# Kernel optimization log

Measured on AMD Instinct MI355X. Metric: run time of the kernel, lower is better.

Reference implementation:

```python
import jax, jax.numpy as jnp
import numpy as np

EPS = 1e-7  # Keras K.epsilon()


def setup_inputs() -> dict:
    key = jax.random.key(0)
    k_x, k_w, k_b, k_u = jax.random.split(key, 4)
    B, T, D, A = 256, 512, 256, 50
    x = jax.random.normal(k_x, (B, T, D), dtype=jnp.float32)
    # Keras initializers.get('normal') -> stddev 0.05 RandomNormal
    W = jax.random.normal(k_w, (D, A), dtype=jnp.float32) * 0.05
    b = jax.random.normal(k_b, (A,), dtype=jnp.float32) * 0.05
    u = jax.random.normal(k_u, (A, 1), dtype=jnp.float32) * 0.05
    return {"x": x, "W": W, "b": b, "u": u}


def reference(x, W, b, u):
    # uit: [B, T, A]
    uit = jnp.tanh(jnp.einsum('btd,da->bta', x, W) + b)
    # ait: [B, T] raw scores -> exp-normalize (as in original, no max-subtract)
    ait = jnp.einsum('bta,a->bt', uit, u[:, 0])
    ait = jnp.exp(ait)
    ait = ait / (jnp.sum(ait, axis=1, keepdims=True) + EPS)
    # weighted pool over time: [B, D]
    return jnp.einsum('btd,bt->bd', x, ait)
```

## Files before the change

### kernel.cpp

```cpp
#include <hip/hip_runtime.h>
#include <math.h>

#define B_  256
#define T_  512
#define D_  256
#define A_  50
#define EPS 1e-7f

typedef short  short8  __attribute__((ext_vector_type(8)));
typedef float  floatx4 __attribute__((ext_vector_type(4)));

__device__ inline unsigned short f2bf(float f) {
    unsigned int u = __float_as_uint(f);
    u = (u + 0x7fffu + ((u >> 16) & 1u)) >> 16;
    return (unsigned short)u;
}

__global__ void prep_kernel(const float* __restrict__ W,
                            const float* __restrict__ bias,
                            const float* __restrict__ u,
                            unsigned short* __restrict__ Wf,
                            float* __restrict__ bu64)
{
    int idx = blockIdx.x * 256 + threadIdx.x;
    int j  = idx & 7;
    int l  = (idx >> 3) & 63;
    int ks = (idx >> 9) & 7;
    int nt = idx >> 12;
    int n  = nt * 16 + (l & 15);
    int k  = ks * 32 + (l >> 4) * 8 + j;
    float val = (n < A_) ? W[k * A_ + n] : 0.0f;
    Wf[idx] = f2bf(val);
    if (idx < 64) {
        bu64[idx]      = (idx < A_) ? bias[idx] : 0.0f;
        bu64[64 + idx] = (idx < A_) ? u[idx]    : 0.0f;
    }
}

__global__ __launch_bounds__(256)
void scores_kernel(const float* __restrict__ x,
                   const unsigned short* __restrict__ Wf,
                   const float* __restrict__ bu64,
                   float* __restrict__ s_out, float* __restrict__ partial)
{
    __shared__ float sred[64];

    const int tid  = threadIdx.x;
    const int w    = tid >> 6;
    const int l    = tid & 63;
    const int c    = l & 15;
    const int quad = l >> 4;
    const size_t rowbase = (size_t)blockIdx.x * 64 + w * 16;

    const float4* __restrict__ xrow = (const float4*)(x + (rowbase + c) * D_);
    const short8* __restrict__ wf8  = (const short8*)Wf;

    float bnc[4], unc[4];
    #pragma unroll
    for (int nt = 0; nt < 4; nt++) {
        bnc[nt] = bu64[nt * 16 + c];
        unc[nt] = bu64[64 + nt * 16 + c];
    }

    floatx4 acc[4];
    #pragma unroll
    for (int nt = 0; nt < 4; nt++) acc[nt] = (floatx4){0.f, 0.f, 0.f, 0.f};

    #pragma unroll
    for (int ks = 0; ks < 8; ks++) {
        const float4 a0 = xrow[ks * 8 + quad * 2];
        const float4 a1 = xrow[ks * 8 + quad * 2 + 1];
        short8 av;
        av[0] = (short)f2bf(a0.x); av[1] = (short)f2bf(a0.y);
        av[2] = (short)f2bf(a0.z); av[3] = (short)f2bf(a0.w);
        av[4] = (short)f2bf(a1.x); av[5] = (short)f2bf(a1.y);
        av[6] = (short)f2bf(a1.z); av[7] = (short)f2bf(a1.w);
        #pragma unroll
        for (int nt = 0; nt < 4; nt++) {
            const short8 bv = wf8[(nt * 8 + ks) * 64 + l];
            acc[nt] = __builtin_amdgcn_mfma_f32_16x16x32_bf16(av, bv, acc[nt], 0, 0, 0);
        }
    }

    float part[4];
    #pragma unroll
    for (int r = 0; r < 4; r++) {
        float v = 0.0f;
        #pragma unroll
        for (int nt = 0; nt < 4; nt++)
            v += tanhf(acc[nt][r] + bnc[nt]) * unc[nt];
        #pragma unroll
        for (int off = 1; off < 16; off <<= 1)
            v += __shfl_xor(v, off, 16);
        part[r] = v;
    }

    if (c == 0) {
        #pragma unroll
        for (int r = 0; r < 4; r++) {
            const float s = expf(part[r]);
            s_out[rowbase + quad * 4 + r] = s;
            sred[w * 16 + quad * 4 + r] = s;
        }
    }
    __syncthreads();
    if (tid == 0) {
        float s = 0.0f;
        #pragma unroll
        for (int i = 0; i < 64; i++) s += sred[i];
        partial[blockIdx.x] = s;
    }
}

__global__ __launch_bounds__(256)
void pool_kernel(const float* __restrict__ x, const float* __restrict__ s_in,
                 const float* __restrict__ partial, float* __restrict__ pp)
{
    __shared__ float s_lds[64];
    __shared__ float part[4 * 256];

    const int tid = threadIdx.x;
    const int bb  = blockIdx.x >> 3;
    const int q   = blockIdx.x & 7;

    float den = EPS;
    #pragma unroll
    for (int i = 0; i < 8; i++) den += partial[bb * 8 + i];
    const float inv = 1.0f / den;

    if (tid < 64)
        s_lds[tid] = s_in[(size_t)bb * T_ + q * 64 + tid] * inv;
    __syncthreads();

    const int w = tid >> 6;
    const int l = tid & 63;

    const float* __restrict__ xb = x + ((size_t)bb * T_ + q * 64) * D_;
    float4 acc = make_float4(0.f, 0.f, 0.f, 0.f);

    #pragma unroll
    for (int i = 0; i < 16; i++) {
        const int t = w * 16 + i;
        float4 xv = *(const float4*)(xb + (size_t)t * D_ + l * 4);
        float sv  = s_lds[t];
        acc.x += xv.x * sv;
        acc.y += xv.y * sv;
        acc.z += xv.z * sv;
        acc.w += xv.w * sv;
    }

    part[w * 256 + l * 4 + 0] = acc.x;
    part[w * 256 + l * 4 + 1] = acc.y;
    part[w * 256 + l * 4 + 2] = acc.z;
    part[w * 256 + l * 4 + 3] = acc.w;
    __syncthreads();

    pp[(size_t)blockIdx.x * 256 + tid] =
        part[tid] + part[256 + tid] + part[512 + tid] + part[768 + tid];
}

__global__ __launch_bounds__(256)
void combine_kernel(const float* __restrict__ pp, float* __restrict__ out)
{
    const size_t idx = (size_t)blockIdx.x * 256 + threadIdx.x;
    const size_t b   = idx >> 8;
    const size_t d   = idx & 255;
    float o = 0.0f;
    #pragma unroll
    for (int q = 0; q < 8; q++) o += pp[(b * 8 + q) * 256 + d];
    out[idx] = o;
}

extern "C" void kernel_launch(void* const* d_in, const int* in_sizes, int n_in,
                              void* d_out, int out_size, void* d_ws, size_t ws_size,
                              hipStream_t stream)
{
    const float* x = (const float*)d_in[0];
    const float* W = (const float*)d_in[1];
    const float* b = (const float*)d_in[2];
    const float* u = (const float*)d_in[3];

    float* scores  = (float*)d_ws;
    float* partial = scores + (size_t)B_ * T_;
    float* bu64    = partial + 2048;
    float* pp      = bu64 + 128;
    unsigned short* Wf = (unsigned short*)(pp + (size_t)B_ * 8 * 256);
    float* out     = (float*)d_out;

    prep_kernel   <<<64,   256, 0, stream>>>(W, b, u, Wf, bu64);
    scores_kernel <<<2048, 256, 0, stream>>>(x, Wf, bu64, scores, partial);
    pool_kernel   <<<2048, 256, 0, stream>>>(x, scores, partial, pp);
    combine_kernel<<<B_,   256, 0, stream>>>(pp, out);
}
```

Measured before the change: 224.4 us.

## Fuse scores, softmax normalization and pooling into one per-batch kernel

Replaces the scores, pool and combine kernels with a single 1024-thread block per batch row. The block computes the attention scores into LDS, reduces the denominator in-block, and pools x while the batch slice is likely still cache-resident. This removes the intermediate score and partial buffers and two launches. In exchange the grid shrinks to 256 blocks, which lowers parallelism, and it adds a serial LDS tree reduction.

```diff
diff --git a/kernel.cpp b/kernel.cpp
--- a/kernel.cpp
+++ b/kernel.cpp
@@ -6,6 +6,7 @@
 #define D_  256
 #define A_  50
 #define EPS 1e-7f
+#define NW  16
 
 typedef short  short8  __attribute__((ext_vector_type(8)));
 typedef float  floatx4 __attribute__((ext_vector_type(4)));
@@ -37,23 +38,24 @@
     }
 }
 
-__global__ __launch_bounds__(256)
-void scores_kernel(const float* __restrict__ x,
-                   const unsigned short* __restrict__ Wf,
-                   const float* __restrict__ bu64,
-                   float* __restrict__ s_out, float* __restrict__ partial)
+__global__ __launch_bounds__(1024)
+void fused_kernel(const float* __restrict__ x,
+                  const unsigned short* __restrict__ Wf,
+                  const float* __restrict__ bu64,
+                  float* __restrict__ out)
 {
-    __shared__ float sred[64];
+    __shared__ float s_lds[T_];
+    __shared__ float part[NW * 256];
 
     const int tid  = threadIdx.x;
     const int w    = tid >> 6;
     const int l    = tid & 63;
     const int c    = l & 15;
     const int quad = l >> 4;
-    const size_t rowbase = (size_t)blockIdx.x * 64 + w * 16;
+    const int bb   = blockIdx.x;
 
-    const float4* __restrict__ xrow = (const float4*)(x + (rowbase + c) * D_);
-    const short8* __restrict__ wf8  = (const short8*)Wf;
+    const float*  __restrict__ xb  = x + (size_t)bb * T_ * D_;
+    const short8* __restrict__ wf8 = (const short8*)Wf;
 
     float bnc[4], unc[4];
     #pragma unroll
@@ -62,113 +64,81 @@
         unc[nt] = bu64[64 + nt * 16 + c];
     }
 
-    floatx4 acc[4];
     #pragma unroll
-    for (int nt = 0; nt < 4; nt++) acc[nt] = (floatx4){0.f, 0.f, 0.f, 0.f};
+    for (int pass = 0; pass < 2; pass++) {
+        const int rowbase = pass * 256 + w * 16;
+        const float4* __restrict__ xrow =
+            (const float4*)(xb + (size_t)(rowbase + c) * D_);
 
-    #pragma unroll
-    for (int ks = 0; ks < 8; ks++) {
-        const float4 a0 = xrow[ks * 8 + quad * 2];
-        const float4 a1 = xrow[ks * 8 + quad * 2 + 1];
-        short8 av;
-        av[0] = (short)f2bf(a0.x); av[1] = (short)f2bf(a0.y);
-        av[2] = (short)f2bf(a0.z); av[3] = (short)f2bf(a0.w);
-        av[4] = (short)f2bf(a1.x); av[5] = (short)f2bf(a1.y);
-        av[6] = (short)f2bf(a1.z); av[7] = (short)f2bf(a1.w);
+        floatx4 acc[4];
         #pragma unroll
-        for (int nt = 0; nt < 4; nt++) {
-            const short8 bv = wf8[(nt * 8 + ks) * 64 + l];
-            acc[nt] = __builtin_amdgcn_mfma_f32_16x16x32_bf16(av, bv, acc[nt], 0, 0, 0);
+        for (int nt = 0; nt < 4; nt++) acc[nt] = (floatx4){0.f, 0.f, 0.f, 0.f};
+
+        #pragma unroll
+        for (int ks = 0; ks < 8; ks++) {
+            const float4 a0 = xrow[ks * 8 + quad * 2];
+            const float4 a1 = xrow[ks * 8 + quad * 2 + 1];
+            short8 av;
+            av[0] = (short)f2bf(a0.x); av[1] = (short)f2bf(a0.y);
+            av[2] = (short)f2bf(a0.z); av[3] = (short)f2bf(a0.w);
+            av[4] = (short)f2bf(a1.x); av[5] = (short)f2bf(a1.y);
+            av[6] = (short)f2bf(a1.z); av[7] = (short)f2bf(a1.w);
+            #pragma unroll
+            for (int nt = 0; nt < 4; nt++) {
+                const short8 bv = wf8[(nt * 8 + ks) * 64 + l];
+                acc[nt] = __builtin_amdgcn_mfma_f32_16x16x32_bf16(av, bv, acc[nt], 0, 0, 0);
+            }
         }
-    }
 
-    float part[4];
-    #pragma unroll
-    for (int r = 0; r < 4; r++) {
-        float v = 0.0f;
-        #pragma unroll
-        for (int nt = 0; nt < 4; nt++)
-            v += tanhf(acc[nt][r] + bnc[nt]) * unc[nt];
-        #pragma unroll
-        for (int off = 1; off < 16; off <<= 1)
-            v += __shfl_xor(v, off, 16);
-        part[r] = v;
-    }
-
-    if (c == 0) {
         #pragma unroll
         for (int r = 0; r < 4; r++) {
-            const float s = expf(part[r]);
-            s_out[rowbase + quad * 4 + r] = s;
-            sred[w * 16 + quad * 4 + r] = s;
+            float v = 0.0f;
+            #pragma unroll
+            for (int nt = 0; nt < 4; nt++)
+                v += tanhf(acc[nt][r] + bnc[nt]) * unc[nt];
+            #pragma unroll
+            for (int off = 1; off < 16; off <<= 1)
+                v += __shfl_xor(v, off, 16);
+            if (c == 0)
+                s_lds[rowbase + quad * 4 + r] = expf(v);
         }
     }
     __syncthreads();
-    if (tid == 0) {
-        float s = 0.0f;
-        #pragma unroll
-        for (int i = 0; i < 64; i++) s += sred[i];
-        partial[blockIdx.x] = s;
+
+    if (tid < 512) part[tid] = s_lds[tid];
+    __syncthreads();
+    for (int off = 256; off > 0; off >>= 1) {
+        if (tid < off) part[tid] += part[tid + off];
+        __syncthreads();
     }
-}
-
-__global__ __launch_bounds__(256)
-void pool_kernel(const float* __restrict__ x, const float* __restrict__ s_in,
-                 const float* __restrict__ partial, float* __restrict__ pp)
-{
-    __shared__ float s_lds[64];
-    __shared__ float part[4 * 256];
-
-    const int tid = threadIdx.x;
-    const int bb  = blockIdx.x >> 3;
-    const int q   = blockIdx.x & 7;
-
-    float den = EPS;
-    #pragma unroll
-    for (int i = 0; i < 8; i++) den += partial[bb * 8 + i];
-    const float inv = 1.0f / den;
-
-    if (tid < 64)
-        s_lds[tid] = s_in[(size_t)bb * T_ + q * 64 + tid] * inv;
+    const float inv = 1.0f / (part[0] + EPS);
     __syncthreads();
 
-    const int w = tid >> 6;
-    const int l = tid & 63;
+    float4 acc2 = make_float4(0.f, 0.f, 0.f, 0.f);
+    const int t0 = w * 32;
+    #pragma unroll
+    for (int i = 0; i < 32; i++) {
+        const float4 xv = *(const float4*)(xb + (size_t)(t0 + i) * D_ + l * 4);
+        const float sv  = s_lds[t0 + i];
+        acc2.x += xv.x * sv;
+        acc2.y += xv.y * sv;
+        acc2.z += xv.z * sv;
+        acc2.w += xv.w * sv;
+    }
+    acc2.x *= inv; acc2.y *= inv; acc2.z *= inv; acc2.w *= inv;
 
-    const float* __restrict__ xb = x + ((size_t)bb * T_ + q * 64) * D_;
-    float4 acc = make_float4(0.f, 0.f, 0.f, 0.f);
-
-    #pragma unroll
-    for (int i = 0; i < 16; i++) {
-        const int t = w * 16 + i;
-        float4 xv = *(const float4*)(xb + (size_t)t * D_ + l * 4);
-        float sv  = s_lds[t];
-        acc.x += xv.x * sv;
-        acc.y += xv.y * sv;
-        acc.z += xv.z * sv;
-        acc.w += xv.w * sv;
-    }
-
-    part[w * 256 + l * 4 + 0] = acc.x;
-    part[w * 256 + l * 4 + 1] = acc.y;
-    part[w * 256 + l * 4 + 2] = acc.z;
-    part[w * 256 + l * 4 + 3] = acc.w;
+    part[w * 256 + l * 4 + 0] = acc2.x;
+    part[w * 256 + l * 4 + 1] = acc2.y;
+    part[w * 256 + l * 4 + 2] = acc2.z;
+    part[w * 256 + l * 4 + 3] = acc2.w;
     __syncthreads();
 
-    pp[(size_t)blockIdx.x * 256 + tid] =
-        part[tid] + part[256 + tid] + part[512 + tid] + part[768 + tid];
-}
-
-__global__ __launch_bounds__(256)
-void combine_kernel(const float* __restrict__ pp, float* __restrict__ out)
-{
-    const size_t idx = (size_t)blockIdx.x * 256 + threadIdx.x;
-    const size_t b   = idx >> 8;
-    const size_t d   = idx & 255;
-    float o = 0.0f;
-    #pragma unroll
-    for (int q = 0; q < 8; q++) o += pp[(b * 8 + q) * 256 + d];
-    out[idx] = o;
+    if (tid < 256) {
+        float o = 0.0f;
+        #pragma unroll
+        for (int wv = 0; wv < NW; wv++) o += part[wv * 256 + tid];
+        out[(size_t)bb * 256 + tid] = o;
+    }
 }
 
 extern "C" void kernel_launch(void* const* d_in, const int* in_sizes, int n_in,
@@ -180,15 +150,10 @@
     const float* b = (const float*)d_in[2];
     const float* u = (const float*)d_in[3];
 
-    float* scores  = (float*)d_ws;
-    float* partial = scores + (size_t)B_ * T_;
-    float* bu64    = partial + 2048;
-    float* pp      = bu64 + 128;
-    unsigned short* Wf = (unsigned short*)(pp + (size_t)B_ * 8 * 256);
-    float* out     = (float*)d_out;
+    unsigned short* Wf  = (unsigned short*)d_ws;
+    float*         bu64 = (float*)(Wf + 16384);
+    float*         out  = (float*)d_out;
 
-    prep_kernel   <<<64,   256, 0, stream>>>(W, b, u, Wf, bu64);
-    scores_kernel <<<2048, 256, 0, stream>>>(x, Wf, bu64, scores, partial);
-    pool_kernel   <<<2048, 256, 0, stream>>>(x, scores, partial, pp);
-    combine_kernel<<<B_,   256, 0, stream>>>(pp, out);
+    prep_kernel  <<<64,  256,  0, stream>>>(W, b, u, Wf, bu64);
+    fused_kernel <<<B_,  1024, 0, stream>>>(x, Wf, bu64, out);
 }
```

After: 219.2 us. 1.02x faster.
